# Performance work log

Measured on AMD Instinct MI355X. Metric: run time of the kernel, lower is better.

## Reference

```python
import jax, jax.numpy as jnp
import numpy as np
import math

B, T, C = 4, 2048, 1024
N_HEAD = 16
HEAD_DIM = C // N_HEAD


def setup_inputs() -> dict:
    key = jax.random.key(0)
    k1, k2, k3, k4, k5 = jax.random.split(key, 5)
    s = 1.0 / math.sqrt(C)
    return {
        "x": jax.random.normal(k1, (B, T, C), dtype=jnp.float32),
        "W_attn": jax.random.normal(k2, (3 * C, C), dtype=jnp.float32) * s,
        "b_attn": jax.random.normal(k3, (3 * C,), dtype=jnp.float32) * 0.02,
        "W_proj": jax.random.normal(k4, (C, C), dtype=jnp.float32) * s,
        "b_proj": jax.random.normal(k5, (C,), dtype=jnp.float32) * 0.02,
    }


def reference(x, W_attn, b_attn, W_proj, b_proj):
    Bx, Tx, Cx = x.shape
    # QKV projection (torch Linear: x @ W.T + b), split into q,k,v
    qkv = jnp.einsum("btc,dc->btd", x, W_attn) + b_attn  # [B,T,3C]
    q, k, v = jnp.split(qkv, 3, axis=-1)
    # [B,T,C] -> [B,H,T,hd]
    def to_heads(t):
        return t.reshape(Bx, Tx, N_HEAD, HEAD_DIM).transpose(0, 2, 1, 3)
    q, k, v = to_heads(q), to_heads(k), to_heads(v)
    scale = 1.0 / math.sqrt(HEAD_DIM)
    att = jnp.einsum("bhqd,bhkd->bhqk", q, k) * scale  # [B,H,T,T]
    causal = jnp.tril(jnp.ones((Tx, Tx), dtype=bool))
    att = jnp.where(causal, att, -jnp.inf)
    att = jax.nn.softmax(att, axis=-1)
    y = jnp.einsum("bhqk,bhkd->bhqd", att, v)  # [B,H,T,hd]
    y = y.transpose(0, 2, 1, 3).reshape(Bx, Tx, Cx)
    y = jnp.einsum("btc,dc->btd", y, W_proj) + b_proj
    return y
```

## Files before the change

### kernel.cpp

```cpp
#include <hip/hip_runtime.h>
#include <hip/hip_bf16.h>
#include <stdint.h>

typedef unsigned short u16;
typedef __attribute__((ext_vector_type(8))) short bf16x8;
typedef __attribute__((ext_vector_type(4))) short s16x4;
typedef __attribute__((ext_vector_type(4))) float f32x4;

#define B_SZ 4
#define T_SZ 2048
#define C_SZ 1024
#define NH   16
#define HD   64
#define LOG2E 1.44269504088896340736f

__device__ __forceinline__ u16 f2bf(float f) {
  unsigned int u = __float_as_uint(f);
  u += 0x7fffu + ((u >> 16) & 1u);
  return (u16)(u >> 16);
}
__device__ __forceinline__ u16 f2bf_hu(float f) {
  return (u16)((__float_as_uint(f) + 0x8000u) >> 16);
}
__device__ __forceinline__ void gload_lds16(const u16* g, u16* l) {
  __builtin_amdgcn_global_load_lds((const __attribute__((address_space(1))) void*)g,
                                   (__attribute__((address_space(3))) void*)l, 16, 0, 0);
}

__global__ void cast3_f32_bf16(const float* __restrict__ x, const float* __restrict__ wa,
                               const float* __restrict__ wp, u16* __restrict__ xb,
                               u16* __restrict__ wab, u16* __restrict__ wpb) {
  const int n1 = 8192 * 1024 / 8, n2 = 3072 * 1024 / 8, n3 = 1024 * 1024 / 8;
  int i = blockIdx.x * blockDim.x + threadIdx.x;
  const float* in; u16* out; int idx;
  if (i < n1)            { in = x;  out = xb;  idx = i; }
  else if (i < n1 + n2)  { in = wa; out = wab; idx = i - n1; }
  else if (i < n1 + n2 + n3) { in = wp; out = wpb; idx = i - n1 - n2; }
  else return;
  const float4* p = (const float4*)in + (size_t)idx * 2;
  float4 a = p[0], b = p[1];
  bf16x8 o;
  o[0] = (short)f2bf(a.x); o[1] = (short)f2bf(a.y);
  o[2] = (short)f2bf(a.z); o[3] = (short)f2bf(a.w);
  o[4] = (short)f2bf(b.x); o[5] = (short)f2bf(b.y);
  o[6] = (short)f2bf(b.z); o[7] = (short)f2bf(b.w);
  ((bf16x8*)out)[idx] = o;
}

__launch_bounds__(256, 3)
__global__ void gemm_bt0(const u16* __restrict__ A, const u16* __restrict__ Bw,
                         const float* __restrict__ bias, float* __restrict__ Cout,
                         int M, int N, int K) {
  __shared__ __align__(16) u16 As[128 * 32];
  __shared__ __align__(16) u16 Bs[128 * 32];
  const int tid = threadIdx.x;
  const int lane = tid & 63;
  const int w = tid >> 6;
  const int wr = w >> 1, wc = w & 1;
  const int quad = lane >> 4, l16 = lane & 15;
  const int m0 = blockIdx.y * 128;
  const int n0 = blockIdx.x * 128;

  const int srow = lane >> 2;
  const int scol = (lane & 3) * 8;
  const u16* gA = A + (size_t)(m0 + w * 32 + srow) * K + scol;
  const u16* gB = Bw + (size_t)(n0 + w * 32 + srow) * K + scol;
  u16* lA0 = &As[(w * 32) * 32];
  u16* lA1 = &As[(w * 32 + 16) * 32];
  u16* lB0 = &Bs[(w * 32) * 32];
  u16* lB1 = &Bs[(w * 32 + 16) * 32];
  const size_t rstep = (size_t)16 * K;

  f32x4 acc[4][4];
#pragma unroll
  for (int i = 0; i < 4; i++)
#pragma unroll
    for (int j = 0; j < 4; j++) acc[i][j] = (f32x4){0.f, 0.f, 0.f, 0.f};

  for (int k0 = 0; k0 < K; k0 += 32) {
    __syncthreads();
    gload_lds16(gA + k0, lA0);
    gload_lds16(gA + rstep + k0, lA1);
    gload_lds16(gB + k0, lB0);
    gload_lds16(gB + rstep + k0, lB1);
    __syncthreads();
    bf16x8 af[4], bfr[4];
#pragma unroll
    for (int mt = 0; mt < 4; mt++)
      af[mt] = *(const bf16x8*)&As[(wr * 64 + mt * 16 + l16) * 32 + quad * 8];
#pragma unroll
    for (int nt = 0; nt < 4; nt++)
      bfr[nt] = *(const bf16x8*)&Bs[(wc * 64 + nt * 16 + l16) * 32 + quad * 8];
#pragma unroll
    for (int mt = 0; mt < 4; mt++)
#pragma unroll
      for (int nt = 0; nt < 4; nt++)
        acc[mt][nt] = __builtin_amdgcn_mfma_f32_16x16x32_bf16(af[mt], bfr[nt], acc[mt][nt], 0, 0, 0);
  }

  float bv[4];
#pragma unroll
  for (int nt = 0; nt < 4; nt++) bv[nt] = bias[n0 + wc * 64 + nt * 16 + l16];
#pragma unroll
  for (int mt = 0; mt < 4; mt++) {
    const int row = m0 + wr * 64 + mt * 16 + quad * 4;
#pragma unroll
    for (int nt = 0; nt < 4; nt++) {
      const int col = n0 + wc * 64 + nt * 16 + l16;
#pragma unroll
      for (int r = 0; r < 4; r++)
        Cout[(size_t)(row + r) * N + col] = acc[mt][nt][r] + bv[nt];
    }
  }
}

__launch_bounds__(512, 2)
__global__ void gemm8_qkv(const u16* __restrict__ A, const u16* __restrict__ Bw,
                          const float* __restrict__ bias,
                          u16* __restrict__ O0, u16* __restrict__ O1, u16* __restrict__ O2,
                          int M, int N, int K) {
  extern __shared__ u16 lds[];
  u16* As = lds;
  u16* Bs = lds + 32768;
  const int tid = threadIdx.x;
  const int lane = tid & 63, w = tid >> 6;
  const int wm = w >> 2, wn = w & 3;
  const int quad = lane >> 4, l16 = lane & 15;

  const int gx = gridDim.x;
  const int nwg = gx * gridDim.y;
  const int wg0 = blockIdx.y * gx + blockIdx.x;
  const int swz = (wg0 & 7) * (nwg >> 3) + (wg0 >> 3);
  const int n0 = (swz % gx) * 256;
  const int m0 = (swz / gx) * 256;

  const int dr8 = lane >> 3;
  const int dc8 = (lane & 7) ^ dr8;
  const u16* gAL = A + (size_t)(m0 + w * 8 + dr8) * K + dc8 * 8;
  const u16* gBL = Bw + (size_t)(n0 + w * 8 + dr8) * K + dc8 * 8;
  u16* dA = As + w * 512;
  u16* dB = Bs + w * 512;

  const int NT = K >> 6;

  auto stageA = [&](int tile) {
    u16* d = dA + (tile & 1) * 16384;
    const u16* g = gAL + (size_t)tile * 64;
#pragma unroll
    for (int h = 0; h < 2; ++h)
#pragma unroll
      for (int i = 0; i < 2; ++i)
        gload_lds16(g + (size_t)(h * 128 + i * 64) * K, d + h * 8192 + i * 4096);
  };
  auto stageB = [&](int tile, int h) {
    u16* d = dB + (tile & 1) * 16384 + h * 8192;
    const u16* g = gBL + (size_t)tile * 64 + (size_t)h * 128 * K;
#pragma unroll
    for (int i = 0; i < 2; ++i)
      gload_lds16(g + (size_t)i * 64 * K, d + i * 4096);
  };

  f32x4 acc[8][4];
#pragma unroll
  for (int i = 0; i < 8; i++)
#pragma unroll
    for (int j = 0; j < 4; j++) acc[i][j] = (f32x4){0.f, 0.f, 0.f, 0.f};

  stageA(0);
  stageB(0, 0); stageB(0, 1);
  stageB(1, 0); stageB(1, 1);
  asm volatile("s_waitcnt vmcnt(4)" ::: "memory");
  __builtin_amdgcn_s_barrier();

  const u16* AbaseR = As + wm * 8192;
  const u16* BbaseR = Bs + (wn >> 1) * 8192 + (wn & 1) * 64 * 64;
  const int sK0 = ((quad) ^ (l16 & 7)) * 8;
  const int sK1 = ((4 + quad) ^ (l16 & 7)) * 8;

  const int NIT = NT >> 1;
  for (int j = 0; j < NIT; ++j) {
#pragma unroll
    for (int tt = 0; tt < 2; ++tt) {
      const int tile = 2 * j + tt;
      const int bufo = (tile & 1) * 16384;
      const u16* Ab = AbaseR + bufo;
      const u16* Bb = BbaseR + bufo;
      bf16x8 bfr[4][2];
#pragma unroll
      for (int mp = 0; mp < 4; ++mp) {
        bf16x8 af[2][2];
#pragma unroll
        for (int a2 = 0; a2 < 2; ++a2) {
          const int ro = ((mp * 2 + a2) * 16 + l16) * 64;
          af[a2][0] = *(const bf16x8*)&Ab[ro + sK0];
          af[a2][1] = *(const bf16x8*)&Ab[ro + sK1];
        }
        if (mp == 0) {
#pragma unroll
          for (int nt = 0; nt < 4; ++nt) {
            const int ro = (nt * 16 + l16) * 64;
            bfr[nt][0] = *(const bf16x8*)&Bb[ro + sK0];
            bfr[nt][1] = *(const bf16x8*)&Bb[ro + sK1];
          }
        }
        if (mp == 0) { if (tile + 1 < NT) stageA(tile + 1); }
        else if (mp == 1) { if (tile + 2 < NT) stageB(tile + 2, 0); }
        else if (mp == 2) { if (tile + 2 < NT) stageB(tile + 2, 1); }
        if (mp == 0) asm volatile("s_waitcnt lgkmcnt(8)");
        asm volatile("" ::: "memory");
        __builtin_amdgcn_s_barrier();
        asm volatile("s_waitcnt lgkmcnt(0)" ::: "memory");
        __builtin_amdgcn_sched_barrier(0);
        __builtin_amdgcn_s_setprio(1);
#pragma unroll
        for (int a2 = 0; a2 < 2; ++a2)
#pragma unroll
          for (int nt = 0; nt < 4; ++nt) {
            f32x4 c = acc[mp * 2 + a2][nt];
            c = __builtin_amdgcn_mfma_f32_16x16x32_bf16(af[a2][0], bfr[nt][0], c, 0, 0, 0);
            c = __builtin_amdgcn_mfma_f32_16x16x32_bf16(af[a2][1], bfr[nt][1], c, 0, 0, 0);
            acc[mp * 2 + a2][nt] = c;
          }
        __builtin_amdgcn_s_setprio(0);
        if (mp == 3) {
          if (tile + 2 >= NT) asm volatile("s_waitcnt vmcnt(0)" ::: "memory");
          else                asm volatile("s_waitcnt vmcnt(4)" ::: "memory");
        }
        asm volatile("" ::: "memory");
        __builtin_amdgcn_s_barrier();
      }
    }
  }

  float bv[4];
#pragma unroll
  for (int nt = 0; nt < 4; nt++) bv[nt] = bias[n0 + wn * 64 + nt * 16 + l16];

  const int nsec = (n0 + wn * 64) >> 10;
  const int hh = ((n0 + wn * 64) >> 6) & 15;
  if (nsec < 2) {
    u16* dst = (nsec == 0 ? O0 : O1);
#pragma unroll
    for (int mt = 0; mt < 8; mt++) {
      const int row = m0 + wm * 128 + mt * 16 + quad * 4;
      const int bb = row >> 11;
      const int t = row & 2047;
#pragma unroll
      for (int nt = 0; nt < 4; nt++) {
        const int dh = nt * 16 + l16;
        const size_t a = (((size_t)bb * NH + hh) * T_SZ + t) * HD + dh;
#pragma unroll
        for (int r = 0; r < 4; r++)
          dst[a + (size_t)r * HD] = f2bf(acc[mt][nt][r] + bv[nt]);
      }
    }
  } else {
    u16* vth = O2;
    u16* S = lds + (size_t)w * (64 * 88);
    const int chunk = lane & 7;
#pragma unroll
    for (int hf = 0; hf < 2; ++hf) {
#pragma unroll
      for (int mt2 = 0; mt2 < 4; ++mt2) {
        const int mt = hf * 4 + mt2;
#pragma unroll
        for (int nt = 0; nt < 4; ++nt) {
          s16x4 pk;
#pragma unroll
          for (int r = 0; r < 4; ++r) pk[r] = (short)f2bf(acc[mt][nt][r] + bv[nt]);
          *(s16x4*)&S[(nt * 16 + l16) * 88 + mt2 * 16 + quad * 4] = pk;
        }
      }
      const int tbase = m0 + wm * 128 + hf * 64;
      const int bb = tbase >> 11;
      const int tb = tbase & 2047;
      const size_t vrow = ((size_t)bb * NH + hh) * HD;
#pragma unroll
      for (int i = 0; i < 8; ++i) {
        const int nr = i * 8 + (lane >> 3);
        bf16x8 vv = *(const bf16x8*)&S[nr * 88 + chunk * 8];
        *(bf16x8*)&vth[(vrow + nr) * T_SZ + tb + chunk * 8] = vv;
      }
    }
  }
}

__device__ __forceinline__ void attn_step(
    int kb, int kbn, int w, int quad, int l16, int qt128, int sw0, int sw1,
    const u16* gK0, const u16* gK1, const u16* gV0, const u16* gV1,
    u16* KsF, u16* VsF, u16* PsW,
    const bf16x8 (&qf)[2][2], f32x4 (&o)[2][4], float (&l_i)[2][4]) {
  __syncthreads();

  if (kb + 1 < kbn) {
    const int nb = (kb + 1) & 1;
    const size_t ko = (size_t)(kb + 1) * 64 * HD;
    const int vo = (kb + 1) * 64;
    gload_lds16(gK0 + ko, KsF + nb * 4096 + (2 * w) * 512);
    gload_lds16(gK1 + ko, KsF + nb * 4096 + (2 * w + 1) * 512);
    gload_lds16(gV0 + vo, VsF + nb * 4096 + (2 * w) * 512);
    gload_lds16(gV1 + vo, VsF + nb * 4096 + (2 * w + 1) * 512);
  }

  const u16* Kb = KsF + (kb & 1) * 4096;
  const u16* Vb = VsF + (kb & 1) * 4096;
  const int kt0 = kb * 64;
  const float SC = 0.125f * LOG2E;

  f32x4 s[2][4];
  __builtin_amdgcn_s_setprio(1);
#pragma unroll
  for (int nt = 0; nt < 4; nt++) {
    bf16x8 kf0 = *(const bf16x8*)&Kb[(nt * 16 + l16) * 64 + sw0];
    bf16x8 kf1 = *(const bf16x8*)&Kb[(nt * 16 + l16) * 64 + sw1];
#pragma unroll
    for (int m = 0; m < 2; m++) {
      f32x4 t0 = (f32x4){0.f, 0.f, 0.f, 0.f};
      t0 = __builtin_amdgcn_mfma_f32_16x16x32_bf16(qf[m][0], kf0, t0, 0, 0, 0);
      t0 = __builtin_amdgcn_mfma_f32_16x16x32_bf16(qf[m][1], kf1, t0, 0, 0, 0);
      s[m][nt] = t0;
    }
  }
  __builtin_amdgcn_s_setprio(0);

  bf16x8 p0a, p1a, p0b, p1b;
#pragma unroll
  for (int m = 0; m < 2; m++) {
    const int mrow = qt128 + w * 32 + m * 16;
    const int qr = mrow + quad * 4;
    const bool diag = (kt0 + 64 > mrow);

    if (diag) {
#pragma unroll
      for (int nt = 0; nt < 4; nt++) {
        const int dk = kt0 + nt * 16 + l16 - qr;
#pragma unroll
        for (int r = 0; r < 4; r++) {
          float v = (dk > r) ? -10000.f : s[m][nt][r] * SC;
          s[m][nt][r] = exp2f(v);
        }
      }
    } else {
#pragma unroll
      for (int nt = 0; nt < 4; nt++)
#pragma unroll
        for (int r = 0; r < 4; r++)
          s[m][nt][r] = exp2f(s[m][nt][r] * SC);
    }
#pragma unroll
    for (int r = 0; r < 4; r++)
      l_i[m][r] += (s[m][0][r] + s[m][1][r]) + (s[m][2][r] + s[m][3][r]);

#pragma unroll
    for (int nt = 0; nt < 4; nt++)
#pragma unroll
      for (int r = 0; r < 4; r++)
        PsW[(quad * 4 + r) * 72 + nt * 16 + l16] = f2bf_hu(s[m][nt][r]);
    if (m == 0) {
      p0a = *(const bf16x8*)&PsW[l16 * 72 + quad * 8];
      p1a = *(const bf16x8*)&PsW[l16 * 72 + 32 + quad * 8];
    } else {
      p0b = *(const bf16x8*)&PsW[l16 * 72 + quad * 8];
      p1b = *(const bf16x8*)&PsW[l16 * 72 + 32 + quad * 8];
    }
  }

  __builtin_amdgcn_s_setprio(1);
#pragma unroll
  for (int nt = 0; nt < 4; nt++) {
    bf16x8 v0 = *(const bf16x8*)&Vb[(nt * 16 + l16) * 64 + sw0];
    bf16x8 v1 = *(const bf16x8*)&Vb[(nt * 16 + l16) * 64 + sw1];
    o[0][nt] = __builtin_amdgcn_mfma_f32_16x16x32_bf16(p0a, v0, o[0][nt], 0, 0, 0);
    o[0][nt] = __builtin_amdgcn_mfma_f32_16x16x32_bf16(p1a, v1, o[0][nt], 0, 0, 0);
    o[1][nt] = __builtin_amdgcn_mfma_f32_16x16x32_bf16(p0b, v0, o[1][nt], 0, 0, 0);
    o[1][nt] = __builtin_amdgcn_mfma_f32_16x16x32_bf16(p1b, v1, o[1][nt], 0, 0, 0);
  }
  __builtin_amdgcn_s_setprio(0);
}

__launch_bounds__(256, 3)
__global__ void attn_fused(const u16* __restrict__ qh, const u16* __restrict__ kh,
                           const u16* __restrict__ vth, u16* __restrict__ out) {
  __shared__ __align__(16) u16 Ks[2][64 * 64];
  __shared__ __align__(16) u16 Vs[2][64 * 64];
  __shared__ __align__(16) u16 Ps[4][16 * 72];
  const int qt = 15 - blockIdx.z;
  const int h = blockIdx.x, b = blockIdx.y;
  const int tid = threadIdx.x;
  const int lane = tid & 63, w = tid >> 6;
  const int quad = lane >> 4, l16 = lane & 15;
  const size_t bh = (size_t)b * NH + h;
  const u16* Kbase = kh + bh * T_SZ * HD;
  const u16* Vbase = vth + bh * HD * T_SZ;
  const int qt128 = qt * 128;

  const int dr = lane >> 3;
  const int dc = (lane & 7) ^ dr;
  const u16* gK0 = Kbase + (size_t)(2 * w * 8 + dr) * HD + dc * 8;
  const u16* gK1 = Kbase + (size_t)((2 * w + 1) * 8 + dr) * HD + dc * 8;
  const u16* gV0 = Vbase + (size_t)(2 * w * 8 + dr) * T_SZ + dc * 8;
  const u16* gV1 = Vbase + (size_t)((2 * w + 1) * 8 + dr) * T_SZ + dc * 8;
  u16* KsF = &Ks[0][0];
  u16* VsF = &Vs[0][0];
  u16* PsW = &Ps[w][0];

  bf16x8 qf[2][2];
#pragma unroll
  for (int m = 0; m < 2; m++) {
    const int t = qt128 + w * 32 + m * 16 + l16;
    const u16* qrow = qh + (bh * T_SZ + t) * HD;
    qf[m][0] = *(const bf16x8*)(qrow + quad * 8);
    qf[m][1] = *(const bf16x8*)(qrow + 32 + quad * 8);
  }

  f32x4 o[2][4];
  float l_i[2][4];
#pragma unroll
  for (int m = 0; m < 2; m++)
#pragma unroll
    for (int i = 0; i < 4; i++) {
      o[m][i] = (f32x4){0.f, 0.f, 0.f, 0.f};
      l_i[m][i] = 0.f;
    }

  const int kbn = 2 * qt + 2;
  const int sw0 = (quad ^ (l16 & 7)) * 8;
  const int sw1 = ((4 + quad) ^ (l16 & 7)) * 8;

  gload_lds16(gK0, KsF + (2 * w) * 512);
  gload_lds16(gK1, KsF + (2 * w + 1) * 512);
  gload_lds16(gV0, VsF + (2 * w) * 512);
  gload_lds16(gV1, VsF + (2 * w + 1) * 512);

  for (int kb = 0; kb < kbn; kb++)
    attn_step(kb, kbn, w, quad, l16, qt128, sw0, sw1,
              gK0, gK1, gV0, gV1, KsF, VsF, PsW, qf, o, l_i);

#pragma unroll
  for (int m = 0; m < 2; m++)
#pragma unroll
    for (int r = 0; r < 4; r++) {
      float v = l_i[m][r];
      v += __shfl_xor(v, 1);
      v += __shfl_xor(v, 2);
      v += __shfl_xor(v, 4);
      v += __shfl_xor(v, 8);
      const float inv = 1.f / v;
      const int t = qt128 + w * 32 + m * 16 + quad * 4 + r;
      const size_t orow = ((size_t)b * T_SZ + t) * C_SZ + (size_t)h * HD;
#pragma unroll
      for (int nt = 0; nt < 4; nt++)
        out[orow + nt * 16 + l16] = f2bf(o[m][nt][r] * inv);
    }
}

extern "C" void kernel_launch(void* const* d_in, const int* in_sizes, int n_in,
                              void* d_out, int out_size, void* d_ws, size_t ws_size,
                              hipStream_t stream) {
  (void)in_sizes; (void)n_in; (void)out_size; (void)ws_size;
  const float* x      = (const float*)d_in[0];
  const float* W_attn = (const float*)d_in[1];
  const float* b_attn = (const float*)d_in[2];
  const float* W_proj = (const float*)d_in[3];
  const float* b_proj = (const float*)d_in[4];
  float* out = (float*)d_out;

  char* ws = (char*)d_ws;
  u16* xb  = (u16*)ws;  ws += (size_t)8192 * 1024 * 2;
  u16* Wab = (u16*)ws;  ws += (size_t)3072 * 1024 * 2;
  u16* Wpb = (u16*)ws;  ws += (size_t)1024 * 1024 * 2;
  u16* qhb = (u16*)ws;  ws += (size_t)8192 * 1024 * 2;
  u16* khb = (u16*)ws;  ws += (size_t)8192 * 1024 * 2;
  u16* vtb = (u16*)ws;  ws += (size_t)8192 * 1024 * 2;
  u16* aob = (u16*)ws;

  dim3 blk(256);
  cast3_f32_bf16<<<6144, blk, 0, stream>>>(x, W_attn, W_proj, xb, Wab, Wpb);

  gemm8_qkv<<<dim3(3072 / 256, 8192 / 256), dim3(512), 131072, stream>>>(
      xb, Wab, b_attn, qhb, khb, vtb, 8192, 3072, 1024);
  attn_fused<<<dim3(NH, B_SZ, 16), blk, 0, stream>>>(qhb, khb, vtb, aob);
  gemm_bt0<<<dim3(1024 / 128, 8192 / 128), blk, 0, stream>>>(
      aob, Wpb, b_proj, out, 8192, 1024, 1024);
}
```

Baseline: 254.4 us.

## Replace output projection GEMM with pipelined 8-wave double-buffered kernel

Swaps the simple 128x128 single-buffered projection GEMM for a 512-thread 256x128-tile kernel. It double-buffers A and B in LDS with XOR-swizzled layout, prefetches the next tiles asynchronously while computing, and uses K=64 steps with split barriers and setprio. The goal is to hide global-load latency, cut LDS bank conflicts and halve the barrier overhead per FLOP. The cost is 96KB of LDS per block, which limits occupancy, plus more fragile hand-written waitcnt scheduling.

Result: faster. 246.5 us (-3.1%).

```diff
diff --git a/kernel.cpp b/kernel.cpp
--- a/kernel.cpp
+++ b/kernel.cpp
@@ -47,73 +47,6 @@
   ((bf16x8*)out)[idx] = o;
 }
 
-__launch_bounds__(256, 3)
-__global__ void gemm_bt0(const u16* __restrict__ A, const u16* __restrict__ Bw,
-                         const float* __restrict__ bias, float* __restrict__ Cout,
-                         int M, int N, int K) {
-  __shared__ __align__(16) u16 As[128 * 32];
-  __shared__ __align__(16) u16 Bs[128 * 32];
-  const int tid = threadIdx.x;
-  const int lane = tid & 63;
-  const int w = tid >> 6;
-  const int wr = w >> 1, wc = w & 1;
-  const int quad = lane >> 4, l16 = lane & 15;
-  const int m0 = blockIdx.y * 128;
-  const int n0 = blockIdx.x * 128;
-
-  const int srow = lane >> 2;
-  const int scol = (lane & 3) * 8;
-  const u16* gA = A + (size_t)(m0 + w * 32 + srow) * K + scol;
-  const u16* gB = Bw + (size_t)(n0 + w * 32 + srow) * K + scol;
-  u16* lA0 = &As[(w * 32) * 32];
-  u16* lA1 = &As[(w * 32 + 16) * 32];
-  u16* lB0 = &Bs[(w * 32) * 32];
-  u16* lB1 = &Bs[(w * 32 + 16) * 32];
-  const size_t rstep = (size_t)16 * K;
-
-  f32x4 acc[4][4];
-#pragma unroll
-  for (int i = 0; i < 4; i++)
-#pragma unroll
-    for (int j = 0; j < 4; j++) acc[i][j] = (f32x4){0.f, 0.f, 0.f, 0.f};
-
-  for (int k0 = 0; k0 < K; k0 += 32) {
-    __syncthreads();
-    gload_lds16(gA + k0, lA0);
-    gload_lds16(gA + rstep + k0, lA1);
-    gload_lds16(gB + k0, lB0);
-    gload_lds16(gB + rstep + k0, lB1);
-    __syncthreads();
-    bf16x8 af[4], bfr[4];
-#pragma unroll
-    for (int mt = 0; mt < 4; mt++)
-      af[mt] = *(const bf16x8*)&As[(wr * 64 + mt * 16 + l16) * 32 + quad * 8];
-#pragma unroll
-    for (int nt = 0; nt < 4; nt++)
-      bfr[nt] = *(const bf16x8*)&Bs[(wc * 64 + nt * 16 + l16) * 32 + quad * 8];
-#pragma unroll
-    for (int mt = 0; mt < 4; mt++)
-#pragma unroll
-      for (int nt = 0; nt < 4; nt++)
-        acc[mt][nt] = __builtin_amdgcn_mfma_f32_16x16x32_bf16(af[mt], bfr[nt], acc[mt][nt], 0, 0, 0);
-  }
-
-  float bv[4];
-#pragma unroll
-  for (int nt = 0; nt < 4; nt++) bv[nt] = bias[n0 + wc * 64 + nt * 16 + l16];
-#pragma unroll
-  for (int mt = 0; mt < 4; mt++) {
-    const int row = m0 + wr * 64 + mt * 16 + quad * 4;
-#pragma unroll
-    for (int nt = 0; nt < 4; nt++) {
-      const int col = n0 + wc * 64 + nt * 16 + l16;
-#pragma unroll
-      for (int r = 0; r < 4; r++)
-        Cout[(size_t)(row + r) * N + col] = acc[mt][nt][r] + bv[nt];
-    }
-  }
-}
-
 __launch_bounds__(512, 2)
 __global__ void gemm8_qkv(const u16* __restrict__ A, const u16* __restrict__ Bw,
                           const float* __restrict__ bias,
@@ -281,6 +214,128 @@
         bf16x8 vv = *(const bf16x8*)&S[nr * 88 + chunk * 8];
         *(bf16x8*)&vth[(vrow + nr) * T_SZ + tb + chunk * 8] = vv;
       }
+    }
+  }
+}
+
+__launch_bounds__(512, 2)
+__global__ void gemm8_proj(const u16* __restrict__ A, const u16* __restrict__ Bw,
+                           const float* __restrict__ bias, float* __restrict__ Cout,
+                           int M, int N, int K) {
+  extern __shared__ u16 lds[];
+  u16* As = lds;
+  u16* Bs = lds + 32768;
+  const int tid = threadIdx.x;
+  const int lane = tid & 63, w = tid >> 6;
+  const int wm = w >> 2, wn = w & 3;
+  const int quad = lane >> 4, l16 = lane & 15;
+
+  const int gx = gridDim.x;
+  const int nwg = gx * gridDim.y;
+  const int wg0 = blockIdx.y * gx + blockIdx.x;
+  const int swz = (wg0 & 7) * (nwg >> 3) + (wg0 >> 3);
+  const int n0 = (swz % gx) * 128;
+  const int m0 = (swz / gx) * 256;
+
+  const int dr8 = lane >> 3;
+  const int dc8 = (lane & 7) ^ dr8;
+  const u16* gAL = A + (size_t)(m0 + w * 8 + dr8) * K + dc8 * 8;
+  const u16* gBL = Bw + (size_t)(n0 + w * 8 + dr8) * K + dc8 * 8;
+  u16* dA = As + w * 512;
+  u16* dB = Bs + w * 512;
+
+  const int NT = K >> 6;
+
+  auto stageA = [&](int tile) {
+    u16* d = dA + (tile & 1) * 16384;
+    const u16* g = gAL + (size_t)tile * 64;
+#pragma unroll
+    for (int sg = 0; sg < 4; ++sg)
+      gload_lds16(g + (size_t)(sg * 64) * K, d + sg * 4096);
+  };
+  auto stageB = [&](int tile) {
+    u16* d = dB + (tile & 1) * 8192;
+    const u16* g = gBL + (size_t)tile * 64;
+#pragma unroll
+    for (int sg = 0; sg < 2; ++sg)
+      gload_lds16(g + (size_t)(sg * 64) * K, d + sg * 4096);
+  };
+
+  f32x4 acc[8][2];
+#pragma unroll
+  for (int i = 0; i < 8; i++)
+#pragma unroll
+    for (int j = 0; j < 2; j++) acc[i][j] = (f32x4){0.f, 0.f, 0.f, 0.f};
+
+  stageA(0); stageB(0); stageB(1);
+  asm volatile("s_waitcnt vmcnt(2)" ::: "memory");
+  __builtin_amdgcn_s_barrier();
+
+  const int sK0 = ((quad) ^ (l16 & 7)) * 8;
+  const int sK1 = ((4 + quad) ^ (l16 & 7)) * 8;
+
+  for (int tile = 0; tile < NT; ++tile) {
+    const u16* Ab = As + (tile & 1) * 16384 + wm * 8192;
+    const u16* Bb = Bs + (tile & 1) * 8192 + wn * 2048;
+    bf16x8 bfr[2][2];
+#pragma unroll
+    for (int mp = 0; mp < 2; ++mp) {
+      bf16x8 af[4][2];
+#pragma unroll
+      for (int a = 0; a < 4; ++a) {
+        const int ro = ((mp * 4 + a) * 16 + l16) * 64;
+        af[a][0] = *(const bf16x8*)&Ab[ro + sK0];
+        af[a][1] = *(const bf16x8*)&Ab[ro + sK1];
+      }
+      if (mp == 0) {
+#pragma unroll
+        for (int nt = 0; nt < 2; ++nt) {
+          const int ro = (nt * 16 + l16) * 64;
+          bfr[nt][0] = *(const bf16x8*)&Bb[ro + sK0];
+          bfr[nt][1] = *(const bf16x8*)&Bb[ro + sK1];
+        }
+        if (tile + 1 < NT) stageA(tile + 1);
+        asm volatile("s_waitcnt lgkmcnt(8)");
+      } else {
+        if (tile + 2 < NT) stageB(tile + 2);
+        asm volatile("s_waitcnt lgkmcnt(4)");
+      }
+      asm volatile("" ::: "memory");
+      __builtin_amdgcn_s_barrier();
+      asm volatile("s_waitcnt lgkmcnt(0)" ::: "memory");
+      __builtin_amdgcn_sched_barrier(0);
+      __builtin_amdgcn_s_setprio(1);
+#pragma unroll
+      for (int a = 0; a < 4; ++a)
+#pragma unroll
+        for (int nt = 0; nt < 2; ++nt) {
+          f32x4 c = acc[mp * 4 + a][nt];
+          c = __builtin_amdgcn_mfma_f32_16x16x32_bf16(af[a][0], bfr[nt][0], c, 0, 0, 0);
+          c = __builtin_amdgcn_mfma_f32_16x16x32_bf16(af[a][1], bfr[nt][1], c, 0, 0, 0);
+          acc[mp * 4 + a][nt] = c;
+        }
+      __builtin_amdgcn_s_setprio(0);
+      if (mp == 1) {
+        if (tile + 2 >= NT) asm volatile("s_waitcnt vmcnt(0)" ::: "memory");
+        else                asm volatile("s_waitcnt vmcnt(2)" ::: "memory");
+      }
+      asm volatile("" ::: "memory");
+      __builtin_amdgcn_s_barrier();
+    }
+  }
+
+  float bv[2];
+#pragma unroll
+  for (int nt = 0; nt < 2; nt++) bv[nt] = bias[n0 + wn * 32 + nt * 16 + l16];
+#pragma unroll
+  for (int mt = 0; mt < 8; mt++) {
+    const int row = m0 + wm * 128 + mt * 16 + quad * 4;
+#pragma unroll
+    for (int nt = 0; nt < 2; nt++) {
+      const int col = n0 + wn * 32 + nt * 16 + l16;
+#pragma unroll
+      for (int r = 0; r < 4; r++)
+        Cout[(size_t)(row + r) * N + col] = acc[mt][nt][r] + bv[nt];
     }
   }
 }
@@ -480,6 +535,6 @@
   gemm8_qkv<<<dim3(3072 / 256, 8192 / 256), dim3(512), 131072, stream>>>(
       xb, Wab, b_attn, qhb, khb, vtb, 8192, 3072, 1024);
   attn_fused<<<dim3(NH, B_SZ, 16), blk, 0, stream>>>(qhb, khb, vtb, aob);
-  gemm_bt0<<<dim3(1024 / 128, 8192 / 128), blk, 0, stream>>>(
+  gemm8_proj<<<dim3(1024 / 128, 8192 / 256), dim3(512), 98304, stream>>>(
       aob, Wpb, b_proj, out, 8192, 1024, 1024);
 }
```
